# Kernel tuning notes

Hardware: AMD Instinct MI355X
Metric: run time of the kernel (lower is better)

Reference implementation:

```python
import jax, jax.numpy as jnp
import numpy as np

B = 16384      # batch
F = 26         # onehot fields
E = 32         # embedding_dim
L = 50         # multihot bag length
V = 1000000    # num_embeddings
CT = 13        # continuous features
D0, D1, D2, D3 = 909, 512, 256, 1
LEAKY = 0.01


def _leaky(x):
    return jnp.where(x >= 0, x, LEAKY * x)


def setup_inputs() -> dict:
    key = jax.random.key(0)
    ks = jax.random.split(key, 16)
    inp = {
        "onehot_i": jax.random.randint(ks[0], (B, F), 0, V),
        "onehot_x": jax.random.uniform(ks[1], (B, F), dtype=jnp.float32),
        "multihot_i1": jax.random.randint(ks[2], (B, L), 0, V),
        "multihot_x1": jax.random.uniform(ks[3], (B, L), dtype=jnp.float32),
        "multihot_i2": jax.random.randint(ks[4], (B, L), 0, V),
        "multihot_x2": jax.random.uniform(ks[5], (B, L), dtype=jnp.float32),
        "ctns": jax.random.normal(ks[6], (B, CT), dtype=jnp.float32),
        # learned parameters
        "wide_table": jax.random.normal(ks[7], (V, 1), dtype=jnp.float32) * 0.02,
        "deep_table": jax.random.normal(ks[8], (V, E), dtype=jnp.float32) * 0.02,
        "w2": jax.random.normal(ks[9], (D1, D0), dtype=jnp.float32) * (1.0 / np.sqrt(D0)),
        "b2": jnp.zeros((D1,), dtype=jnp.float32),
        "w3": jax.random.normal(ks[10], (D2, D1), dtype=jnp.float32) * (1.0 / np.sqrt(D1)),
        "b3": jnp.zeros((D2,), dtype=jnp.float32),
        "w4": jax.random.normal(ks[11], (D3, D2), dtype=jnp.float32) * (1.0 / np.sqrt(D2)),
        "b4": jnp.zeros((D3,), dtype=jnp.float32),
    }
    return inp


def reference(onehot_i, onehot_x, multihot_i1, multihot_x1, multihot_i2,
              multihot_x2, ctns, wide_table, deep_table, w2, b2, w3, b3, w4, b4):
    # ---- wide part ----
    # Original broadcasts the [B,F,1] wide embedding against x repeated E times,
    # then sums over all columns. That equals E * sum_f(w[idx]*x).
    wide_sum = (wide_table[onehot_i, 0] * onehot_x).sum(axis=1)          # [B]
    wide_sum = wide_sum + (wide_table[multihot_i1, 0] * multihot_x1).sum(axis=1)
    wide_sum = wide_sum + (wide_table[multihot_i2, 0] * multihot_x2).sum(axis=1)
    wide_out = E * wide_sum                                              # [B]

    # ---- deep part: gather, scale by field weight, pool multihot bags ----
    d_one = (deep_table[onehot_i] * onehot_x[:, :, None]).reshape(B, F * E)   # [B, F*E]
    d_m1 = (deep_table[multihot_i1] * multihot_x1[:, :, None]).sum(axis=1)    # [B, E]
    d_m2 = (deep_table[multihot_i2] * multihot_x2[:, :, None]).sum(axis=1)    # [B, E]
    x = jnp.concatenate([d_one, d_m1, d_m2, ctns], axis=1)                    # [B, D0]

    # dropout p=0.0 (deterministic reference)
    x = _leaky(x @ w2.T + b2)
    x = _leaky(x @ w3.T + b3)
    x = (x @ w4.T + b4).squeeze(-1)                                           # [B]
    return jax.nn.sigmoid(x + wide_out)
```

## Files before the change

kernel.cpp:

```cpp
#include <hip/hip_runtime.h>
#include <hip/hip_bf16.h>
#include <math.h>

#define B_    16384
#define F_    26
#define E_    32
#define L_    50
#define CT_   13
#define D0_   909
#define D0P   928
#define D1_   512
#define D2_   256

#define NEMB  4096
#define W2N   (D1_ * D0P)
#define W3N   (D2_ * D1_)
#define CVTB  ((W2N + W3N + 255) / 256)

typedef __bf16 bf16x8 __attribute__((ext_vector_type(8)));
typedef float f32x4 __attribute__((ext_vector_type(4)));

__device__ inline unsigned short f2b(float f) {
    union { __hip_bfloat16 h; unsigned short u; } v;
    v.h = __float2bfloat16(f);
    return v.u;
}
__device__ inline void gld_lds16(const void* g, void* l) {
    __builtin_amdgcn_global_load_lds(
        (const __attribute__((address_space(1))) unsigned int*)g,
        (__attribute__((address_space(3))) unsigned int*)l, 16, 0, 0);
}

__global__ __launch_bounds__(256) void embed_cvt_kernel(
    const int* __restrict__ oi, const float* __restrict__ ox,
    const int* __restrict__ i1, const float* __restrict__ x1,
    const int* __restrict__ i2, const float* __restrict__ x2,
    const float* __restrict__ ct, const float* __restrict__ wtab,
    const float* __restrict__ dtab,
    const float* __restrict__ w2, const float* __restrict__ w3,
    __hip_bfloat16* __restrict__ x0b, float* __restrict__ wid,
    __hip_bfloat16* __restrict__ w2b, __hip_bfloat16* __restrict__ w3b)
{
    const int tid  = threadIdx.x;
    const int lane = tid & 63;
    const int w    = tid >> 6;

    if (blockIdx.x >= NEMB) {
        int i = (blockIdx.x - NEMB) * 256 + tid;
        if (i < W2N) {
            int r = i / D0P, c = i - r * D0P;
            float v = (c < D0_) ? w2[r * D0_ + c] : 0.f;
            w2b[i] = __float2bfloat16(v);
        } else {
            int j = i - W2N;
            if (j < W3N) w3b[j] = __float2bfloat16(w3[j]);
        }
        return;
    }

    const int s = blockIdx.x * 4 + w;
    const int g = lane >> 3;
    const int l = lane & 7;
    unsigned short* xrow = (unsigned short*)(x0b + (size_t)s * D0P);
    const f32x4* dt4 = (const f32x4*)dtab;

    int koh[4]; float soh[4];
#pragma unroll
    for (int t = 0; t < 4; t++) {
        int f = g + 8 * t; bool v = (f < F_);
        koh[t] = v ? oi[s * F_ + f] : 0;
        soh[t] = v ? ox[s * F_ + f] : 0.f;
    }
    int k1[7], k2[7]; float sc1[7], sc2[7];
#pragma unroll
    for (int t = 0; t < 7; t++) {
        int j = g + 8 * t; bool v = (j < L_);
        k1[t]  = v ? i1[s * L_ + j] : 0;
        sc1[t] = v ? x1[s * L_ + j] : 0.f;
        k2[t]  = v ? i2[s * L_ + j] : 0;
        sc2[t] = v ? x2[s * L_ + j] : 0.f;
    }
    f32x4 r1[7], r2[7], roh[4];
#pragma unroll
    for (int t = 0; t < 7; t++) r1[t] = dt4[(size_t)k1[t] * 8 + l];
#pragma unroll
    for (int t = 0; t < 7; t++) r2[t] = dt4[(size_t)k2[t] * 8 + l];
#pragma unroll
    for (int t = 0; t < 4; t++) roh[t] = dt4[(size_t)koh[t] * 8 + l];

#pragma unroll
    for (int t = 0; t < 4; t++) {
        int f = g + 8 * t;
        if (f < F_) {
            ushort4 o;
            o.x = f2b(roh[t].x * soh[t]); o.y = f2b(roh[t].y * soh[t]);
            o.z = f2b(roh[t].z * soh[t]); o.w = f2b(roh[t].w * soh[t]);
            *(ushort4*)(xrow + f * E_ + l * 4) = o;
        }
    }
    f32x4 a1 = {0.f,0.f,0.f,0.f}, a2 = {0.f,0.f,0.f,0.f};
#pragma unroll
    for (int t = 0; t < 7; t++) {
        a1.x = fmaf(r1[t].x, sc1[t], a1.x); a1.y = fmaf(r1[t].y, sc1[t], a1.y);
        a1.z = fmaf(r1[t].z, sc1[t], a1.z); a1.w = fmaf(r1[t].w, sc1[t], a1.w);
        a2.x = fmaf(r2[t].x, sc2[t], a2.x); a2.y = fmaf(r2[t].y, sc2[t], a2.y);
        a2.z = fmaf(r2[t].z, sc2[t], a2.z); a2.w = fmaf(r2[t].w, sc2[t], a2.w);
    }
#pragma unroll
    for (int m = 8; m < 64; m <<= 1) {
        a1.x += __shfl_xor(a1.x, m); a1.y += __shfl_xor(a1.y, m);
        a1.z += __shfl_xor(a1.z, m); a1.w += __shfl_xor(a1.w, m);
        a2.x += __shfl_xor(a2.x, m); a2.y += __shfl_xor(a2.y, m);
        a2.z += __shfl_xor(a2.z, m); a2.w += __shfl_xor(a2.w, m);
    }
    if (g == 0) {
        ushort4 o; o.x = f2b(a1.x); o.y = f2b(a1.y); o.z = f2b(a1.z); o.w = f2b(a1.w);
        *(ushort4*)(xrow + F_ * E_ + l * 4) = o;
    }
    if (g == 1) {
        ushort4 o; o.x = f2b(a2.x); o.y = f2b(a2.y); o.z = f2b(a2.z); o.w = f2b(a2.w);
        *(ushort4*)(xrow + F_ * E_ + E_ + l * 4) = o;
    }
    if (lane < E_) {
        float v = (lane < CT_) ? ct[s * CT_ + lane] : 0.f;
        xrow[F_ * E_ + 2 * E_ + lane] = f2b(v);
    }
    float acc = 0.f;
#pragma unroll
    for (int t = lane; t < F_ + 2 * L_; t += 64) {
        int idx; float xv;
        if (t < F_)            { idx = oi[s * F_ + t];           xv = ox[s * F_ + t]; }
        else if (t < F_ + L_)  { int j = t - F_;      idx = i1[s * L_ + j]; xv = x1[s * L_ + j]; }
        else                   { int j = t - F_ - L_; idx = i2[s * L_ + j]; xv = x2[s * L_ + j]; }
        acc += wtab[idx] * xv;
    }
    for (int o = 32; o; o >>= 1) acc += __shfl_xor(acc, o);
    if (lane == 0) wid[s] = (float)E_ * acc;
}

__global__ __launch_bounds__(512, 2) void mlp_kernel(
    const __hip_bfloat16* __restrict__ x0b,
    const __hip_bfloat16* __restrict__ w2b, const float* __restrict__ b2,
    const __hip_bfloat16* __restrict__ w3b, const float* __restrict__ b3,
    const float* __restrict__ w4, const float* __restrict__ b4,
    const float* __restrict__ wid, float* __restrict__ out)
{
    __shared__ __align__(16) __hip_bfloat16 stageA[64 * 32];
    __shared__ __align__(16) __hip_bfloat16 stageB[512 * 32];
    __shared__ __align__(16) unsigned short h1s[16 * 64 * 40];
    __shared__ float parts[8 * 64];

    const int tid  = threadIdx.x;
    const int lane = tid & 63;
    const int w    = tid >> 6;
    const int r0   = blockIdx.x * 64;
    const int fr   = lane & 15;
    const int kq   = lane >> 4;
    const int kg8  = kq * 8;
    const int srow = lane >> 2;
    const int scol = (lane & 3) * 8;

    f32x4 acc[4][4] = {};
    for (int ks = 0; ks < 29; ks++) {
        if (lane < 32)
            gld_lds16(x0b + (size_t)(r0 + w * 8 + (lane >> 2)) * D0P + ks * 32 + scol,
                      (char*)stageA + w * 512);
#pragma unroll
        for (int r = 0; r < 4; r++)
            gld_lds16(w2b + (size_t)(w * 64 + r * 16 + srow) * D0P + ks * 32 + scol,
                      (char*)stageB + w * 4096 + r * 1024);
        __syncthreads();

        bf16x8 af[4], bfv[4];
#pragma unroll
        for (int i = 0; i < 4; i++)
            af[i] = *(const bf16x8*)(stageA + (i * 16 + fr) * 32 + kg8);
#pragma unroll
        for (int j = 0; j < 4; j++)
            bfv[j] = *(const bf16x8*)(stageB + (w * 64 + j * 16 + fr) * 32 + kg8);
#pragma unroll
        for (int i = 0; i < 4; i++)
#pragma unroll
            for (int j = 0; j < 4; j++)
                acc[i][j] = __builtin_amdgcn_mfma_f32_16x16x32_bf16(af[i], bfv[j], acc[i][j], 0, 0, 0);
        __syncthreads();
    }

#pragma unroll
    for (int j = 0; j < 4; j++) {
        const int n   = w * 64 + j * 16 + fr;
        const float bb = b2[n];
        const int ksl = w * 2 + (j >> 1);
        const int kk  = (j & 1) * 16 + fr;
#pragma unroll
        for (int i = 0; i < 4; i++)
#pragma unroll
            for (int r = 0; r < 4; r++) {
                const int row = i * 16 + kq * 4 + r;
                float v = acc[i][j][r] + bb;
                v = (v >= 0.f) ? v : 0.01f * v;
                h1s[ksl * 2560 + row * 40 + kk] = f2b(v);
            }
    }
    __syncthreads();

    f32x4 acc2[4][2] = {};
    for (int ks = 0; ks < 16; ks++) {
#pragma unroll
        for (int r = 0; r < 2; r++)
            gld_lds16(w3b + (size_t)(w * 32 + r * 16 + srow) * D1_ + ks * 32 + scol,
                      (char*)stageB + w * 2048 + r * 1024);
        __syncthreads();

        bf16x8 af[4], bfv[2];
#pragma unroll
        for (int i = 0; i < 4; i++)
            af[i] = *(const bf16x8*)(h1s + ks * 2560 + (i * 16 + fr) * 40 + kg8);
#pragma unroll
        for (int j = 0; j < 2; j++)
            bfv[j] = *(const bf16x8*)(stageB + (w * 32 + j * 16 + fr) * 32 + kg8);
#pragma unroll
        for (int i = 0; i < 4; i++)
#pragma unroll
            for (int j = 0; j < 2; j++)
                acc2[i][j] = __builtin_amdgcn_mfma_f32_16x16x32_bf16(af[i], bfv[j], acc2[i][j], 0, 0, 0);
        __syncthreads();
    }

    float p[4][4];
#pragma unroll
    for (int i = 0; i < 4; i++)
#pragma unroll
        for (int r = 0; r < 4; r++) p[i][r] = 0.f;
#pragma unroll
    for (int j = 0; j < 2; j++) {
        const int n = w * 32 + j * 16 + fr;
        const float bb = b3[n];
        const float wv = w4[n];
#pragma unroll
        for (int i = 0; i < 4; i++)
#pragma unroll
            for (int r = 0; r < 4; r++) {
                float v = acc2[i][j][r] + bb;
                v = (v >= 0.f) ? v : 0.01f * v;
                p[i][r] = fmaf(v, wv, p[i][r]);
            }
    }
#pragma unroll
    for (int m = 1; m < 16; m <<= 1)
#pragma unroll
        for (int i = 0; i < 4; i++)
#pragma unroll
            for (int r = 0; r < 4; r++) p[i][r] += __shfl_xor(p[i][r], m);
    if (fr == 0) {
#pragma unroll
        for (int i = 0; i < 4; i++)
#pragma unroll
            for (int r = 0; r < 4; r++)
                parts[w * 64 + i * 16 + kq * 4 + r] = p[i][r];
    }
    __syncthreads();
    if (tid < 64) {
        float x = b4[0] + wid[r0 + tid];
#pragma unroll
        for (int ww = 0; ww < 8; ww++) x += parts[ww * 64 + tid];
        out[r0 + tid] = 1.f / (1.f + expf(-x));
    }
}

extern "C" void kernel_launch(void* const* d_in, const int* in_sizes, int n_in,
                              void* d_out, int out_size, void* d_ws, size_t ws_size,
                              hipStream_t stream) {
    const int*   oi  = (const int*)  d_in[0];
    const float* ox  = (const float*)d_in[1];
    const int*   i1  = (const int*)  d_in[2];
    const float* x1  = (const float*)d_in[3];
    const int*   i2  = (const int*)  d_in[4];
    const float* x2  = (const float*)d_in[5];
    const float* ct  = (const float*)d_in[6];
    const float* wt  = (const float*)d_in[7];
    const float* dt  = (const float*)d_in[8];
    const float* w2  = (const float*)d_in[9];
    const float* b2  = (const float*)d_in[10];
    const float* w3  = (const float*)d_in[11];
    const float* b3  = (const float*)d_in[12];
    const float* w4  = (const float*)d_in[13];
    const float* b4  = (const float*)d_in[14];
    float* out = (float*)d_out;

    char* ws = (char*)d_ws;
    __hip_bfloat16* x0b = (__hip_bfloat16*)(ws);
    float*          wid = (float*)         (ws + 30408704);
    __hip_bfloat16* w2b = (__hip_bfloat16*)(ws + 30474240);
    __hip_bfloat16* w3b = (__hip_bfloat16*)(ws + 31424512);

    embed_cvt_kernel<<<NEMB + CVTB, 256, 0, stream>>>(
        oi, ox, i1, x1, i2, x2, ct, wt, dt, w2, w3, x0b, wid, w2b, w3b);
    mlp_kernel<<<B_ / 64, 512, 0, stream>>>(x0b, w2b, b2, w3b, b3, w4, b4, wid, out);
}
```

Baseline: 126.2 us.

## Pad K to 960 and process 64-wide K chunks per barrier in MLP

Pads the first layer's K dimension from 928 to 960 so each main-loop iteration stages two 32-wide K slices into double LDS buffers. This halves the number of loop iterations and __syncthreads barriers in both GEMM phases. The hidden-activation LDS buffer is relaid out as unpadded 32-column chunks, which may cause LDS bank conflicts on reads. The change also adds padded zero MACs and drops the min-blocks launch bound.

After: 120.7 us. 4.3% less time.

```diff
diff --git a/kernel.cpp b/kernel.cpp
--- a/kernel.cpp
+++ b/kernel.cpp
@@ -8,12 +8,12 @@
 #define L_    50
 #define CT_   13
 #define D0_   909
-#define D0P   928
+#define KP    960
 #define D1_   512
 #define D2_   256
 
 #define NEMB  4096
-#define W2N   (D1_ * D0P)
+#define W2N   (D1_ * KP)
 #define W3N   (D2_ * D1_)
 #define CVTB  ((W2N + W3N + 255) / 256)
 
@@ -48,7 +48,7 @@
     if (blockIdx.x >= NEMB) {
         int i = (blockIdx.x - NEMB) * 256 + tid;
         if (i < W2N) {
-            int r = i / D0P, c = i - r * D0P;
+            int r = i / KP, c = i - r * KP;
             float v = (c < D0_) ? w2[r * D0_ + c] : 0.f;
             w2b[i] = __float2bfloat16(v);
         } else {
@@ -61,7 +61,7 @@
     const int s = blockIdx.x * 4 + w;
     const int g = lane >> 3;
     const int l = lane & 7;
-    unsigned short* xrow = (unsigned short*)(x0b + (size_t)s * D0P);
+    unsigned short* xrow = (unsigned short*)(x0b + (size_t)s * KP);
     const f32x4* dt4 = (const f32x4*)dtab;
 
     int koh[4]; float soh[4];
@@ -121,7 +121,7 @@
         ushort4 o; o.x = f2b(a2.x); o.y = f2b(a2.y); o.z = f2b(a2.z); o.w = f2b(a2.w);
         *(ushort4*)(xrow + F_ * E_ + E_ + l * 4) = o;
     }
-    if (lane < E_) {
+    {
         float v = (lane < CT_) ? ct[s * CT_ + lane] : 0.f;
         xrow[F_ * E_ + 2 * E_ + lane] = f2b(v);
     }
@@ -138,17 +138,17 @@
     if (lane == 0) wid[s] = (float)E_ * acc;
 }
 
-__global__ __launch_bounds__(512, 2) void mlp_kernel(
+__global__ __launch_bounds__(512) void mlp_kernel(
     const __hip_bfloat16* __restrict__ x0b,
     const __hip_bfloat16* __restrict__ w2b, const float* __restrict__ b2,
     const __hip_bfloat16* __restrict__ w3b, const float* __restrict__ b3,
     const float* __restrict__ w4, const float* __restrict__ b4,
     const float* __restrict__ wid, float* __restrict__ out)
 {
-    __shared__ __align__(16) __hip_bfloat16 stageA[64 * 32];
-    __shared__ __align__(16) __hip_bfloat16 stageB[512 * 32];
-    __shared__ __align__(16) unsigned short h1s[16 * 64 * 40];
-    __shared__ float parts[8 * 64];
+    __shared__ __align__(16) __hip_bfloat16 As[2][64 * 32];
+    __shared__ __align__(16) __hip_bfloat16 Bs[2][512 * 32];
+    __shared__ __align__(16) unsigned short h1s[16][64 * 32];
+    __shared__ float parts[512];
 
     const int tid  = threadIdx.x;
     const int lane = tid & 63;
@@ -156,42 +156,50 @@
     const int r0   = blockIdx.x * 64;
     const int fr   = lane & 15;
     const int kq   = lane >> 4;
-    const int kg8  = kq * 8;
+    const int kg   = kq * 8;
     const int srow = lane >> 2;
     const int scol = (lane & 3) * 8;
 
     f32x4 acc[4][4] = {};
-    for (int ks = 0; ks < 29; ks++) {
-        if (lane < 32)
-            gld_lds16(x0b + (size_t)(r0 + w * 8 + (lane >> 2)) * D0P + ks * 32 + scol,
-                      (char*)stageA + w * 512);
-#pragma unroll
-        for (int r = 0; r < 4; r++)
-            gld_lds16(w2b + (size_t)(w * 64 + r * 16 + srow) * D0P + ks * 32 + scol,
-                      (char*)stageB + w * 4096 + r * 1024);
+    for (int k0 = 0; k0 < KP; k0 += 64) {
+        {
+            const int p = w >> 2;
+            const int rbase = (w & 3) * 16;
+            gld_lds16(x0b + (size_t)(r0 + rbase + srow) * KP + k0 + p * 32 + scol,
+                      (char*)As + p * 4096 + rbase * 64);
+        }
+#pragma unroll
+        for (int p = 0; p < 2; p++)
+#pragma unroll
+            for (int rr = 0; rr < 4; rr++)
+                gld_lds16(w2b + (size_t)(w * 64 + rr * 16 + srow) * KP + k0 + p * 32 + scol,
+                          (char*)Bs + p * 32768 + (w * 64 + rr * 16) * 64);
         __syncthreads();
 
-        bf16x8 af[4], bfv[4];
-#pragma unroll
-        for (int i = 0; i < 4; i++)
-            af[i] = *(const bf16x8*)(stageA + (i * 16 + fr) * 32 + kg8);
-#pragma unroll
-        for (int j = 0; j < 4; j++)
-            bfv[j] = *(const bf16x8*)(stageB + (w * 64 + j * 16 + fr) * 32 + kg8);
-#pragma unroll
-        for (int i = 0; i < 4; i++)
+#pragma unroll
+        for (int p = 0; p < 2; p++) {
+            bf16x8 af[4], bfv[4];
+#pragma unroll
+            for (int i = 0; i < 4; i++)
+                af[i] = *(const bf16x8*)(As[p] + (i * 16 + fr) * 32 + kg);
 #pragma unroll
             for (int j = 0; j < 4; j++)
-                acc[i][j] = __builtin_amdgcn_mfma_f32_16x16x32_bf16(af[i], bfv[j], acc[i][j], 0, 0, 0);
+                bfv[j] = *(const bf16x8*)(Bs[p] + (w * 64 + j * 16 + fr) * 32 + kg);
+#pragma unroll
+            for (int i = 0; i < 4; i++)
+#pragma unroll
+                for (int j = 0; j < 4; j++)
+                    acc[i][j] = __builtin_amdgcn_mfma_f32_16x16x32_bf16(af[i], bfv[j], acc[i][j], 0, 0, 0);
+        }
         __syncthreads();
     }
 
 #pragma unroll
     for (int j = 0; j < 4; j++) {
-        const int n   = w * 64 + j * 16 + fr;
+        const int n  = w * 64 + j * 16 + fr;
         const float bb = b2[n];
-        const int ksl = w * 2 + (j >> 1);
-        const int kk  = (j & 1) * 16 + fr;
+        const int chunk = n >> 5;
+        const int kk    = n & 31;
 #pragma unroll
         for (int i = 0; i < 4; i++)
 #pragma unroll
@@ -199,39 +207,45 @@
                 const int row = i * 16 + kq * 4 + r;
                 float v = acc[i][j][r] + bb;
                 v = (v >= 0.f) ? v : 0.01f * v;
-                h1s[ksl * 2560 + row * 40 + kk] = f2b(v);
+                h1s[chunk][row * 32 + kk] = f2b(v);
             }
     }
     __syncthreads();
 
     f32x4 acc2[4][2] = {};
-    for (int ks = 0; ks < 16; ks++) {
-#pragma unroll
-        for (int r = 0; r < 2; r++)
-            gld_lds16(w3b + (size_t)(w * 32 + r * 16 + srow) * D1_ + ks * 32 + scol,
-                      (char*)stageB + w * 2048 + r * 1024);
+    for (int q = 0; q < 8; q++) {
+#pragma unroll
+        for (int p = 0; p < 2; p++)
+#pragma unroll
+            for (int rr = 0; rr < 2; rr++)
+                gld_lds16(w3b + (size_t)(w * 32 + rr * 16 + srow) * D1_ + q * 64 + p * 32 + scol,
+                          (char*)Bs + p * 16384 + (w * 32 + rr * 16) * 64);
         __syncthreads();
 
-        bf16x8 af[4], bfv[2];
-#pragma unroll
-        for (int i = 0; i < 4; i++)
-            af[i] = *(const bf16x8*)(h1s + ks * 2560 + (i * 16 + fr) * 40 + kg8);
-#pragma unroll
-        for (int j = 0; j < 2; j++)
-            bfv[j] = *(const bf16x8*)(stageB + (w * 32 + j * 16 + fr) * 32 + kg8);
-#pragma unroll
-        for (int i = 0; i < 4; i++)
+#pragma unroll
+        for (int p = 0; p < 2; p++) {
+            const __hip_bfloat16* Bp = (const __hip_bfloat16*)((char*)Bs + p * 16384);
+            bf16x8 af[4], bfv[2];
+#pragma unroll
+            for (int i = 0; i < 4; i++)
+                af[i] = *(const bf16x8*)(&h1s[2 * q + p][(i * 16 + fr) * 32 + kg]);
 #pragma unroll
             for (int j = 0; j < 2; j++)
-                acc2[i][j] = __builtin_amdgcn_mfma_f32_16x16x32_bf16(af[i], bfv[j], acc2[i][j], 0, 0, 0);
+                bfv[j] = *(const bf16x8*)(Bp + (w * 32 + j * 16 + fr) * 32 + kg);
+#pragma unroll
+            for (int i = 0; i < 4; i++)
+#pragma unroll
+                for (int j = 0; j < 2; j++)
+                    acc2[i][j] = __builtin_amdgcn_mfma_f32_16x16x32_bf16(af[i], bfv[j], acc2[i][j], 0, 0, 0);
+        }
         __syncthreads();
     }
 
-    float p[4][4];
+    float p4[4][4];
 #pragma unroll
     for (int i = 0; i < 4; i++)
 #pragma unroll
-        for (int r = 0; r < 4; r++) p[i][r] = 0.f;
+        for (int r = 0; r < 4; r++) p4[i][r] = 0.f;
 #pragma unroll
     for (int j = 0; j < 2; j++) {
         const int n = w * 32 + j * 16 + fr;
@@ -243,7 +257,7 @@
             for (int r = 0; r < 4; r++) {
                 float v = acc2[i][j][r] + bb;
                 v = (v >= 0.f) ? v : 0.01f * v;
-                p[i][r] = fmaf(v, wv, p[i][r]);
+                p4[i][r] = fmaf(v, wv, p4[i][r]);
             }
     }
 #pragma unroll
@@ -251,13 +265,13 @@
 #pragma unroll
         for (int i = 0; i < 4; i++)
 #pragma unroll
-            for (int r = 0; r < 4; r++) p[i][r] += __shfl_xor(p[i][r], m);
+            for (int r = 0; r < 4; r++) p4[i][r] += __shfl_xor(p4[i][r], m);
     if (fr == 0) {
 #pragma unroll
         for (int i = 0; i < 4; i++)
 #pragma unroll
             for (int r = 0; r < 4; r++)
-                parts[w * 64 + i * 16 + kq * 4 + r] = p[i][r];
+                parts[w * 64 + i * 16 + kq * 4 + r] = p4[i][r];
     }
     __syncthreads();
     if (tid < 64) {
@@ -290,9 +304,9 @@
 
     char* ws = (char*)d_ws;
     __hip_bfloat16* x0b = (__hip_bfloat16*)(ws);
-    float*          wid = (float*)         (ws + 30408704);
-    __hip_bfloat16* w2b = (__hip_bfloat16*)(ws + 30474240);
-    __hip_bfloat16* w3b = (__hip_bfloat16*)(ws + 31424512);
+    float*          wid = (float*)         (ws + 31457280);
+    __hip_bfloat16* w2b = (__hip_bfloat16*)(ws + 31522816);
+    __hip_bfloat16* w3b = (__hip_bfloat16*)(ws + 32505856);
 
     embed_cvt_kernel<<<NEMB + CVTB, 256, 0, stream>>>(
         oi, ox, i1, x1, i2, x2, ct, wt, dt, w2, w3, x0b, wid, w2b, w3b);
```
